# Performance work log

Hardware: AMD Instinct MI355X
Metric: run time of the kernel (lower is better)

The kernel has to match this reference:

```python
import jax, jax.numpy as jnp
import numpy as np

N_GAUSS = 2048
FOCAL = 110.0
NEAR = 0.3
EPS = 1e-4  # matches EPS in source (scale.abs() + EPS)
LOWPASS = 0.3 / (FOCAL * FOCAL)  # low-pass dilation in camera-plane units


def _q2r(q):
    # q: (N,4) wxyz -> (N,3,3) rotation matrices (normalized quaternions)
    q = q / (jnp.linalg.norm(q, axis=-1, keepdims=True) + 1e-8)
    w, x, y, z = q[:, 0], q[:, 1], q[:, 2], q[:, 3]
    R = jnp.stack([
        jnp.stack([1 - 2 * (y * y + z * z), 2 * (x * y - w * z), 2 * (x * z + w * y)], -1),
        jnp.stack([2 * (x * y + w * z), 1 - 2 * (x * x + z * z), 2 * (y * z - w * x)], -1),
        jnp.stack([2 * (x * z - w * y), 2 * (y * z + w * x), 1 - 2 * (x * x + y * y)], -1),
    ], axis=1)
    return R


def _forward(pos, rgb, opa, quat, scale, w2c, tran, H, W):
    # world -> camera
    cam = pos @ w2c.T + tran                      # (N,3)
    z = cam[:, 2]
    valid = z > NEAR
    zs = jnp.where(valid, z, 1.0)
    u = cam[:, 0] / zs                            # camera-plane x
    v = cam[:, 1] / zs                            # camera-plane y

    # 3D covariance: RSSR^T  (scale_activation='abs')
    R = _q2r(quat)
    s = jnp.abs(scale) + EPS
    RS = R * s[:, None, :]                        # R @ diag(s)
    cov3 = jnp.einsum('nij,nkj->nik', RS, RS)     # (N,3,3)
    # rotate into camera frame: W cov3 W^T
    covc = jnp.einsum('ij,njk,lk->nil', w2c, cov3, w2c)

    # perspective Jacobian, 2D covariance = J covc J^T
    iz = 1.0 / zs
    zero = jnp.zeros_like(iz)
    J = jnp.stack([
        jnp.stack([iz, zero, -u * iz], -1),
        jnp.stack([zero, iz, -v * iz], -1),
    ], axis=1)                                    # (N,2,3)
    cov2 = jnp.einsum('nij,njk,nlk->nil', J, covc, J)
    a = cov2[:, 0, 0] + LOWPASS
    b = cov2[:, 0, 1]
    c = cov2[:, 1, 1] + LOWPASS
    det = jnp.maximum(a * c - b * b, 1e-12)
    ia, ib, ic = c / det, -b / det, a / det       # inverse 2x2 cov

    # global front-to-back depth sort (invalid gaussians pushed to the end)
    order = jnp.argsort(jnp.where(valid, z, jnp.inf))
    u, v = u[order], v[order]
    ia, ib, ic = ia[order], ib[order], ic[order]
    opa_s = opa[order]
    rgb_s = rgb[order]
    valid_s = valid[order]

    # pixel centers in camera-plane units
    upix = (jnp.arange(W, dtype=jnp.float32) - W / 2 + 0.5) / FOCAL
    vpix = (jnp.arange(H, dtype=jnp.float32) - H / 2 + 0.5) / FOCAL
    gu, gv = jnp.meshgrid(upix, vpix)             # (H,W) each
    gu = gu.reshape(-1)                           # (P,)
    gv = gv.reshape(-1)

    dx = gu[None, :] - u[:, None]                 # (N,P)
    dy = gv[None, :] - v[:, None]
    power = -0.5 * (ia[:, None] * dx * dx + 2.0 * ib[:, None] * dx * dy + ic[:, None] * dy * dy)
    gw = jnp.exp(jnp.minimum(power, 0.0))
    alpha = jnp.clip(jax.nn.sigmoid(opa_s)[:, None] * gw, 0.0, 0.99)
    alpha = jnp.where(valid_s[:, None], alpha, 0.0)

    # transmittance via exclusive cumsum of log(1-alpha), front-to-back
    lt = jnp.log1p(-alpha)
    logT = jnp.cumsum(lt, axis=0) - lt            # exclusive prefix sum
    wgt = alpha * jnp.exp(logT)                   # (N,P) compositing weights
    img = jnp.einsum('np,nc->pc', wgt, jax.nn.sigmoid(rgb_s))
    return img.reshape(H, W, 3)


def setup_inputs() -> dict:
    key = jax.random.key(0)
    k = jax.random.split(key, 8)
    H, W = 128, 128
    # positions in front of the (near-identity) camera, inside the frustum
    z = jax.random.uniform(k[0], (N_GAUSS,), minval=2.0, maxval=6.0)
    uv = jax.random.uniform(k[1], (N_GAUSS, 2), minval=-0.5, maxval=0.5)
    pos = jnp.stack([uv[:, 0] * z, uv[:, 1] * z, z], axis=-1)
    rgb = jax.random.normal(k[2], (N_GAUSS, 3), dtype=jnp.float32)
    opa = jax.random.normal(k[3], (N_GAUSS,), dtype=jnp.float32)
    quat = jax.random.normal(k[4], (N_GAUSS, 4), dtype=jnp.float32)
    scale = jax.random.uniform(k[5], (N_GAUSS, 3), minval=0.005, maxval=0.05)
    # small random rotation (Rodrigues) so w2c is a valid, near-identity rotation
    axis = jax.random.normal(k[6], (3,))
    axis = axis / (jnp.linalg.norm(axis) + 1e-8)
    th = 0.05
    K = jnp.array([[0.0, -axis[2], axis[1]],
                   [axis[2], 0.0, -axis[0]],
                   [-axis[1], axis[0], 0.0]], dtype=jnp.float32)
    w2c = jnp.eye(3, dtype=jnp.float32) + jnp.sin(th) * K + (1 - jnp.cos(th)) * (K @ K)
    tran = 0.01 * jax.random.normal(k[7], (3,), dtype=jnp.float32)
    return {"pos": pos, "rgb": rgb, "opa": opa, "quat": quat, "scale": scale,
            "w2c": w2c, "tran": tran, "H": H, "W": W}


def reference(pos, rgb, opa, quat, scale, w2c, tran, H, W):
    return _forward(pos, rgb, opa, quat, scale, w2c, tran, H, W)
```

## Files before the change

kernel.cpp:

```cpp
#include <hip/hip_runtime.h>
#include <hip/hip_fp16.h>
#include <math.h>

#define NG 2048
#define HH 128
#define WW 128
#define FOCAL 110.0f
#define NEARP 0.3f
#define EPSS 1e-4f
#define LOWPASS (0.3f / (110.0f * 110.0f))
#define L2E 1.4426950408889634f
#define INV_L2E 0.6931471805599453f
#define LN_INV_ACUT 11.512925465f

#define NSEG 16

#define EXP2F(x) __builtin_amdgcn_exp2f(x)
#define LOG2F(x) __builtin_amdgcn_logf(x)
#define RCPF(x)  __builtin_amdgcn_rcpf(x)
#define SQRTF(x) __builtin_amdgcn_sqrtf(x)

struct Proj {
    float u, v, a, b, c, z, osig;
    bool valid;
};

__device__ __forceinline__ Proj project_one(int g,
        const float* __restrict__ pos, const float* __restrict__ opa,
        const float* __restrict__ quat, const float* __restrict__ scale,
        const float* __restrict__ w2c, const float* __restrict__ tran) {
    float W00 = w2c[0], W01 = w2c[1], W02 = w2c[2];
    float W10 = w2c[3], W11 = w2c[4], W12 = w2c[5];
    float W20 = w2c[6], W21 = w2c[7], W22 = w2c[8];

    float px = pos[g * 3 + 0], py = pos[g * 3 + 1], pz = pos[g * 3 + 2];
    float cx = W00 * px + W01 * py + W02 * pz + tran[0];
    float cy = W10 * px + W11 * py + W12 * pz + tran[1];
    float cz = W20 * px + W21 * py + W22 * pz + tran[2];

    bool valid = cz > NEARP;
    float iz = valid ? RCPF(cz) : 1.0f;
    float u = cx * iz;
    float v = cy * iz;

    float qw = quat[g * 4 + 0], qx = quat[g * 4 + 1], qy = quat[g * 4 + 2], qz = quat[g * 4 + 3];
    float qq = qw * qw + qx * qx + qy * qy + qz * qz;
    float inv = RCPF(SQRTF(qq) + 1e-8f);
    qw *= inv; qx *= inv; qy *= inv; qz *= inv;
    float R00 = 1.0f - 2.0f * (qy * qy + qz * qz);
    float R01 = 2.0f * (qx * qy - qw * qz);
    float R02 = 2.0f * (qx * qz + qw * qy);
    float R10 = 2.0f * (qx * qy + qw * qz);
    float R11 = 1.0f - 2.0f * (qx * qx + qz * qz);
    float R12 = 2.0f * (qy * qz - qw * qx);
    float R20 = 2.0f * (qx * qz - qw * qy);
    float R21 = 2.0f * (qy * qz + qw * qx);
    float R22 = 1.0f - 2.0f * (qx * qx + qy * qy);

    float s0 = fabsf(scale[g * 3 + 0]) + EPSS;
    float s1 = fabsf(scale[g * 3 + 1]) + EPSS;
    float s2 = fabsf(scale[g * 3 + 2]) + EPSS;

    float A00 = R00 * s0, A01 = R01 * s1, A02 = R02 * s2;
    float A10 = R10 * s0, A11 = R11 * s1, A12 = R12 * s2;
    float A20 = R20 * s0, A21 = R21 * s1, A22 = R22 * s2;
    float C00 = A00 * A00 + A01 * A01 + A02 * A02;
    float C01 = A00 * A10 + A01 * A11 + A02 * A12;
    float C02 = A00 * A20 + A01 * A21 + A02 * A22;
    float C11 = A10 * A10 + A11 * A11 + A12 * A12;
    float C12 = A10 * A20 + A11 * A21 + A12 * A22;
    float C22 = A20 * A20 + A21 * A21 + A22 * A22;

    float B00 = W00 * C00 + W01 * C01 + W02 * C02;
    float B01 = W00 * C01 + W01 * C11 + W02 * C12;
    float B02 = W00 * C02 + W01 * C12 + W02 * C22;
    float B10 = W10 * C00 + W11 * C01 + W12 * C02;
    float B11 = W10 * C01 + W11 * C11 + W12 * C12;
    float B12 = W10 * C02 + W11 * C12 + W12 * C22;
    float B20 = W20 * C00 + W21 * C01 + W22 * C02;
    float B21 = W20 * C01 + W21 * C11 + W22 * C12;
    float B22 = W20 * C02 + W21 * C12 + W22 * C22;
    float M00 = B00 * W00 + B01 * W01 + B02 * W02;
    float M01 = B00 * W10 + B01 * W11 + B02 * W12;
    float M02 = B00 * W20 + B01 * W21 + B02 * W22;
    float M11 = B10 * W10 + B11 * W11 + B12 * W12;
    float M12 = B10 * W20 + B11 * W21 + B12 * W22;
    float M22 = B20 * W20 + B21 * W21 + B22 * W22;

    float iz2 = iz * iz;
    Proj r;
    r.a = iz2 * (M00 - 2.0f * u * M02 + u * u * M22) + LOWPASS;
    r.b = iz2 * (M01 - v * M02 - u * M12 + u * v * M22);
    r.c = iz2 * (M11 - 2.0f * v * M12 + v * v * M22) + LOWPASS;
    r.u = u; r.v = v; r.z = cz; r.valid = valid;
    float e = EXP2F(-opa[g] * L2E);
    r.osig = valid ? RCPF(1.0f + e) : 0.0f;
    return r;
}

__device__ __forceinline__ float fast_sigmoid(float x) {
    return RCPF(1.0f + EXP2F(-x * L2E));
}

__global__ __launch_bounds__(1024) void splat_fused(const float* __restrict__ pos,
                                                    const float* __restrict__ rgb,
                                                    const float* __restrict__ opa,
                                                    const float* __restrict__ quat,
                                                    const float* __restrict__ scale,
                                                    const float* __restrict__ w2c,
                                                    const float* __restrict__ tran,
                                                    float* __restrict__ out) {
    __shared__ unsigned long long zk[NG];
    __shared__ unsigned short srt[NG];
    __shared__ float4 ppA[NG];
    __shared__ float4 ppB[NG];
    __shared__ float4 seg[NSEG][64];
    __shared__ int cnt;

    int t = threadIdx.x;
    int lane = t & 63;
    int wave = t >> 6;
    int bx = blockIdx.x & 15, by = blockIdx.x >> 4;

    float cu = ((float)(bx * 8) + 3.5f - 63.5f) / FOCAL;
    float cv = ((float)(by * 8) + 3.5f - 63.5f) / FOCAL;
    const float hw = 3.5f / FOCAL;

    if (t == 0) cnt = 0;
    __syncthreads();

    #pragma unroll
    for (int part = 0; part < 2; ++part) {
        int g = t + part * 1024;
        Proj P = project_one(g, pos, opa, quat, scale, w2c, tran);
        float e = EXP2F(-opa[g] * L2E);
        float tau = 2.0f * (LN_INV_ACUT - LOG2F(1.0f + e) * INV_L2E);
        bool survive = false;
        if (P.valid && tau > 0.0f) {
            float ru = SQRTF(tau * P.a);
            float rv = SQRTF(tau * P.c);
            survive = (fabsf(P.u - cu) <= ru + hw) && (fabsf(P.v - cv) <= rv + hw);
        }
        if (survive) {
            int s = atomicAdd(&cnt, 1);
            zk[s] = ((unsigned long long)__float_as_uint(P.z) << 32) | (unsigned int)g;
        }
    }
    __syncthreads();
    int L = cnt;

    for (int i = t; i < L; i += 1024) {
        unsigned long long ki = zk[i];
        int r = 0;
        #pragma unroll 4
        for (int j = 0; j < L; ++j) r += (zk[j] < ki) ? 1 : 0;
        srt[r] = (unsigned short)(ki & 0xffffu);
    }
    __syncthreads();

    for (int i = t; i < L; i += 1024) {
        int g = srt[i];
        Proj P = project_one(g, pos, opa, quat, scale, w2c, tran);
        float det = fmaxf(P.a * P.c - P.b * P.b, 1e-12f);
        float idet = RCPF(det);
        float Af = -0.5f * L2E * (P.c * idet);
        float Bf =  L2E * (P.b * idet);
        float Cf = -0.5f * L2E * (P.a * idet);
        float rr = fast_sigmoid(rgb[g * 3 + 0]);
        float gg = fast_sigmoid(rgb[g * 3 + 1]);
        float bb = fast_sigmoid(rgb[g * 3 + 2]);
        union { __half2 h; float f; } prg, pb;
        prg.h = __floats2half2_rn(rr, gg);
        pb.h  = __floats2half2_rn(bb, 0.0f);
        ppA[i] = make_float4(P.u, P.v, Af, Bf);
        ppB[i] = make_float4(Cf, P.osig, prg.f, pb.f);
    }
    __syncthreads();

    int px = bx * 8 + (lane & 7);
    int py = by * 8 + (lane >> 3);
    float gu = ((float)px - 63.5f) / FOCAL;
    float gv = ((float)py - 63.5f) / FOCAL;

    int s = (L * wave) >> 4;
    int e = (L * (wave + 1)) >> 4;

    float T = 1.0f, cr = 0.0f, cg = 0.0f, cb = 0.0f;
    for (int i = s; i < e; ++i) {
        float4 q0 = ppA[i];
        float4 q1 = ppB[i];

        float dx = gu - q0.x;
        float dy = gv - q0.y;
        float t1 = fmaf(q0.w, dy, q0.z * dx);
        float p  = fmaf(t1, dx, q1.x * (dy * dy));
        p = fminf(p, 0.0f);
        float gw = EXP2F(p);
        float alpha = fminf(q1.y * gw, 0.99f);
        float w = alpha * T;

        union { float f; __half2 h; } crg, cbb;
        crg.f = q1.z; cbb.f = q1.w;
        float2 rg = __half22float2(crg.h);
        float bch = __low2float(cbb.h);

        cr = fmaf(w, rg.x, cr);
        cg = fmaf(w, rg.y, cg);
        cb = fmaf(w, bch, cb);
        T = fmaf(-alpha, T, T);
    }
    seg[wave][lane] = make_float4(cr, cg, cb, T);
    __syncthreads();

    if (t < 64) {
        float Tt = 1.0f, r = 0.0f, g = 0.0f, b = 0.0f;
        #pragma unroll
        for (int sgi = 0; sgi < NSEG; ++sgi) {
            float4 v = seg[sgi][t];
            r = fmaf(Tt, v.x, r);
            g = fmaf(Tt, v.y, g);
            b = fmaf(Tt, v.z, b);
            Tt *= v.w;
        }
        int p = py * WW + px;
        out[p * 3 + 0] = r;
        out[p * 3 + 1] = g;
        out[p * 3 + 2] = b;
    }
}

extern "C" void kernel_launch(void* const* d_in, const int* in_sizes, int n_in,
                              void* d_out, int out_size, void* d_ws, size_t ws_size,
                              hipStream_t stream) {
    const float* pos   = (const float*)d_in[0];
    const float* rgb   = (const float*)d_in[1];
    const float* opa   = (const float*)d_in[2];
    const float* quat  = (const float*)d_in[3];
    const float* scale = (const float*)d_in[4];
    const float* w2c   = (const float*)d_in[5];
    const float* tran  = (const float*)d_in[6];
    float* out = (float*)d_out;

    splat_fused<<<(HH * WW) / 64, 1024, 0, stream>>>(pos, rgb, opa, quat, scale, w2c, tran, out);
}
```

Measured before the change: 12.64 us.

## Compute projected 2D covariance directly and parallelize depth rank sort

The 2D covariance is now built directly from the product of the perspective Jacobian, w2c, rotation and scale, instead of forming the full 3D covariance and rotating it. The per-gaussian conic parameters are computed once, during culling, and written to shared memory at the atomic slot, so surviving gaussians are no longer projected a second time. The rank sort now has 16 lanes share each key and sum their counts with shuffles, which spreads the quadratic comparison work when few gaussians survive. The cost is an extra indirection in the render loop: each iteration first reads the sorted slot from srt, then loads that gaussian's parameters.

```diff
diff --git a/kernel.cpp b/kernel.cpp
--- a/kernel.cpp
+++ b/kernel.cpp
@@ -18,85 +18,6 @@
 #define EXP2F(x) __builtin_amdgcn_exp2f(x)
 #define LOG2F(x) __builtin_amdgcn_logf(x)
 #define RCPF(x)  __builtin_amdgcn_rcpf(x)
-#define SQRTF(x) __builtin_amdgcn_sqrtf(x)
-
-struct Proj {
-    float u, v, a, b, c, z, osig;
-    bool valid;
-};
-
-__device__ __forceinline__ Proj project_one(int g,
-        const float* __restrict__ pos, const float* __restrict__ opa,
-        const float* __restrict__ quat, const float* __restrict__ scale,
-        const float* __restrict__ w2c, const float* __restrict__ tran) {
-    float W00 = w2c[0], W01 = w2c[1], W02 = w2c[2];
-    float W10 = w2c[3], W11 = w2c[4], W12 = w2c[5];
-    float W20 = w2c[6], W21 = w2c[7], W22 = w2c[8];
-
-    float px = pos[g * 3 + 0], py = pos[g * 3 + 1], pz = pos[g * 3 + 2];
-    float cx = W00 * px + W01 * py + W02 * pz + tran[0];
-    float cy = W10 * px + W11 * py + W12 * pz + tran[1];
-    float cz = W20 * px + W21 * py + W22 * pz + tran[2];
-
-    bool valid = cz > NEARP;
-    float iz = valid ? RCPF(cz) : 1.0f;
-    float u = cx * iz;
-    float v = cy * iz;
-
-    float qw = quat[g * 4 + 0], qx = quat[g * 4 + 1], qy = quat[g * 4 + 2], qz = quat[g * 4 + 3];
-    float qq = qw * qw + qx * qx + qy * qy + qz * qz;
-    float inv = RCPF(SQRTF(qq) + 1e-8f);
-    qw *= inv; qx *= inv; qy *= inv; qz *= inv;
-    float R00 = 1.0f - 2.0f * (qy * qy + qz * qz);
-    float R01 = 2.0f * (qx * qy - qw * qz);
-    float R02 = 2.0f * (qx * qz + qw * qy);
-    float R10 = 2.0f * (qx * qy + qw * qz);
-    float R11 = 1.0f - 2.0f * (qx * qx + qz * qz);
-    float R12 = 2.0f * (qy * qz - qw * qx);
-    float R20 = 2.0f * (qx * qz - qw * qy);
-    float R21 = 2.0f * (qy * qz + qw * qx);
-    float R22 = 1.0f - 2.0f * (qx * qx + qy * qy);
-
-    float s0 = fabsf(scale[g * 3 + 0]) + EPSS;
-    float s1 = fabsf(scale[g * 3 + 1]) + EPSS;
-    float s2 = fabsf(scale[g * 3 + 2]) + EPSS;
-
-    float A00 = R00 * s0, A01 = R01 * s1, A02 = R02 * s2;
-    float A10 = R10 * s0, A11 = R11 * s1, A12 = R12 * s2;
-    float A20 = R20 * s0, A21 = R21 * s1, A22 = R22 * s2;
-    float C00 = A00 * A00 + A01 * A01 + A02 * A02;
-    float C01 = A00 * A10 + A01 * A11 + A02 * A12;
-    float C02 = A00 * A20 + A01 * A21 + A02 * A22;
-    float C11 = A10 * A10 + A11 * A11 + A12 * A12;
-    float C12 = A10 * A20 + A11 * A21 + A12 * A22;
-    float C22 = A20 * A20 + A21 * A21 + A22 * A22;
-
-    float B00 = W00 * C00 + W01 * C01 + W02 * C02;
-    float B01 = W00 * C01 + W01 * C11 + W02 * C12;
-    float B02 = W00 * C02 + W01 * C12 + W02 * C22;
-    float B10 = W10 * C00 + W11 * C01 + W12 * C02;
-    float B11 = W10 * C01 + W11 * C11 + W12 * C12;
-    float B12 = W10 * C02 + W11 * C12 + W12 * C22;
-    float B20 = W20 * C00 + W21 * C01 + W22 * C02;
-    float B21 = W20 * C01 + W21 * C11 + W22 * C12;
-    float B22 = W20 * C02 + W21 * C12 + W22 * C22;
-    float M00 = B00 * W00 + B01 * W01 + B02 * W02;
-    float M01 = B00 * W10 + B01 * W11 + B02 * W12;
-    float M02 = B00 * W20 + B01 * W21 + B02 * W22;
-    float M11 = B10 * W10 + B11 * W11 + B12 * W12;
-    float M12 = B10 * W20 + B11 * W21 + B12 * W22;
-    float M22 = B20 * W20 + B21 * W21 + B22 * W22;
-
-    float iz2 = iz * iz;
-    Proj r;
-    r.a = iz2 * (M00 - 2.0f * u * M02 + u * u * M22) + LOWPASS;
-    r.b = iz2 * (M01 - v * M02 - u * M12 + u * v * M22);
-    r.c = iz2 * (M11 - 2.0f * v * M12 + v * v * M22) + LOWPASS;
-    r.u = u; r.v = v; r.z = cz; r.valid = valid;
-    float e = EXP2F(-opa[g] * L2E);
-    r.osig = valid ? RCPF(1.0f + e) : 0.0f;
-    return r;
-}
 
 __device__ __forceinline__ float fast_sigmoid(float x) {
     return RCPF(1.0f + EXP2F(-x * L2E));
@@ -105,15 +26,15 @@
 __global__ __launch_bounds__(1024) void splat_fused(const float* __restrict__ pos,
                                                     const float* __restrict__ rgb,
                                                     const float* __restrict__ opa,
-                                                    const float* __restrict__ quat,
+                                                    const float4* __restrict__ quat,
                                                     const float* __restrict__ scale,
                                                     const float* __restrict__ w2c,
                                                     const float* __restrict__ tran,
                                                     float* __restrict__ out) {
     __shared__ unsigned long long zk[NG];
-    __shared__ unsigned short srt[NG];
     __shared__ float4 ppA[NG];
     __shared__ float4 ppB[NG];
+    __shared__ unsigned short srt[NG];
     __shared__ float4 seg[NSEG][64];
     __shared__ int cnt;
 
@@ -129,51 +50,106 @@
     if (t == 0) cnt = 0;
     __syncthreads();
 
+    float W00 = w2c[0], W01 = w2c[1], W02 = w2c[2];
+    float W10 = w2c[3], W11 = w2c[4], W12 = w2c[5];
+    float W20 = w2c[6], W21 = w2c[7], W22 = w2c[8];
+    float t0 = tran[0], t1 = tran[1], t2 = tran[2];
+
     #pragma unroll
     for (int part = 0; part < 2; ++part) {
         int g = t + part * 1024;
-        Proj P = project_one(g, pos, opa, quat, scale, w2c, tran);
+
+        float px = pos[g * 3 + 0], py = pos[g * 3 + 1], pz = pos[g * 3 + 2];
+        float cx = W00 * px + W01 * py + W02 * pz + t0;
+        float cy = W10 * px + W11 * py + W12 * pz + t1;
+        float cz = W20 * px + W21 * py + W22 * pz + t2;
+
+        bool valid = cz > NEARP;
+        float iz = valid ? RCPF(cz) : 1.0f;
+        float u = cx * iz;
+        float v = cy * iz;
+
         float e = EXP2F(-opa[g] * L2E);
+        float osig = RCPF(1.0f + e);
         float tau = 2.0f * (LN_INV_ACUT - LOG2F(1.0f + e) * INV_L2E);
-        bool survive = false;
-        if (P.valid && tau > 0.0f) {
-            float ru = SQRTF(tau * P.a);
-            float rv = SQRTF(tau * P.c);
-            survive = (fabsf(P.u - cu) <= ru + hw) && (fabsf(P.v - cv) <= rv + hw);
+
+        float k00 = iz * (W00 - u * W20), k01 = iz * (W01 - u * W21), k02 = iz * (W02 - u * W22);
+        float k10 = iz * (W10 - v * W20), k11 = iz * (W11 - v * W21), k12 = iz * (W12 - v * W22);
+
+        float4 q = quat[g];
+        float qw = q.x, qx = q.y, qy = q.z, qz = q.w;
+        float qq = qw * qw + qx * qx + qy * qy + qz * qz;
+        float inv = RCPF(__builtin_amdgcn_sqrtf(qq) + 1e-8f);
+        qw *= inv; qx *= inv; qy *= inv; qz *= inv;
+        float R00 = 1.0f - 2.0f * (qy * qy + qz * qz);
+        float R01 = 2.0f * (qx * qy - qw * qz);
+        float R02 = 2.0f * (qx * qz + qw * qy);
+        float R10 = 2.0f * (qx * qy + qw * qz);
+        float R11 = 1.0f - 2.0f * (qx * qx + qz * qz);
+        float R12 = 2.0f * (qy * qz - qw * qx);
+        float R20 = 2.0f * (qx * qz - qw * qy);
+        float R21 = 2.0f * (qy * qz + qw * qx);
+        float R22 = 1.0f - 2.0f * (qx * qx + qy * qy);
+
+        float s0 = fabsf(scale[g * 3 + 0]) + EPSS;
+        float s1 = fabsf(scale[g * 3 + 1]) + EPSS;
+        float s2 = fabsf(scale[g * 3 + 2]) + EPSS;
+
+        float g00 = (k00 * R00 + k01 * R10 + k02 * R20) * s0;
+        float g01 = (k00 * R01 + k01 * R11 + k02 * R21) * s1;
+        float g02 = (k00 * R02 + k01 * R12 + k02 * R22) * s2;
+        float g10 = (k10 * R00 + k11 * R10 + k12 * R20) * s0;
+        float g11 = (k10 * R01 + k11 * R11 + k12 * R21) * s1;
+        float g12 = (k10 * R02 + k11 * R12 + k12 * R22) * s2;
+
+        float a = g00 * g00 + g01 * g01 + g02 * g02 + LOWPASS;
+        float c = g10 * g10 + g11 * g11 + g12 * g12 + LOWPASS;
+
+        float du = fmaxf(fabsf(u - cu) - hw, 0.0f);
+        float dv = fmaxf(fabsf(v - cv) - hw, 0.0f);
+        bool survive = valid && (tau > 0.0f) &&
+                       (du * du <= tau * a) && (dv * dv <= tau * c);
+
+        if (survive) {
+            float b = g00 * g10 + g01 * g11 + g02 * g12;
+            float det = fmaxf(a * c - b * b, 1e-12f);
+            float idet = RCPF(det);
+            float Af = -0.5f * L2E * (c * idet);
+            float Bf =  L2E * (b * idet);
+            float Cf = -0.5f * L2E * (a * idet);
+            int s = atomicAdd(&cnt, 1);
+            zk[s] = ((unsigned long long)__float_as_uint(cz) << 32) | (unsigned int)g;
+            ppA[s] = make_float4(u, v, Af, Bf);
+            ppB[s] = make_float4(Cf, osig, 0.0f, 0.0f);
         }
-        if (survive) {
-            int s = atomicAdd(&cnt, 1);
-            zk[s] = ((unsigned long long)__float_as_uint(P.z) << 32) | (unsigned int)g;
+    }
+    __syncthreads();
+    int L = cnt;
+
+    {
+        int sub = t & 15;
+        for (int i = t >> 4; i < L; i += 64) {
+            unsigned long long ki = zk[i];
+            int r = 0;
+            for (int j = sub; j < L; j += 16) r += (zk[j] < ki) ? 1 : 0;
+            r += __shfl_xor(r, 1);
+            r += __shfl_xor(r, 2);
+            r += __shfl_xor(r, 4);
+            r += __shfl_xor(r, 8);
+            if (sub == 0) srt[r] = (unsigned short)i;
         }
     }
-    __syncthreads();
-    int L = cnt;
 
     for (int i = t; i < L; i += 1024) {
-        unsigned long long ki = zk[i];
-        int r = 0;
-        #pragma unroll 4
-        for (int j = 0; j < L; ++j) r += (zk[j] < ki) ? 1 : 0;
-        srt[r] = (unsigned short)(ki & 0xffffu);
-    }
-    __syncthreads();
-
-    for (int i = t; i < L; i += 1024) {
-        int g = srt[i];
-        Proj P = project_one(g, pos, opa, quat, scale, w2c, tran);
-        float det = fmaxf(P.a * P.c - P.b * P.b, 1e-12f);
-        float idet = RCPF(det);
-        float Af = -0.5f * L2E * (P.c * idet);
-        float Bf =  L2E * (P.b * idet);
-        float Cf = -0.5f * L2E * (P.a * idet);
+        int g = (int)(zk[i] & 0xffffu);
         float rr = fast_sigmoid(rgb[g * 3 + 0]);
         float gg = fast_sigmoid(rgb[g * 3 + 1]);
         float bb = fast_sigmoid(rgb[g * 3 + 2]);
         union { __half2 h; float f; } prg, pb;
         prg.h = __floats2half2_rn(rr, gg);
         pb.h  = __floats2half2_rn(bb, 0.0f);
-        ppA[i] = make_float4(P.u, P.v, Af, Bf);
-        ppB[i] = make_float4(Cf, P.osig, prg.f, pb.f);
+        ppB[i].z = prg.f;
+        ppB[i].w = pb.f;
     }
     __syncthreads();
 
@@ -187,13 +163,14 @@
 
     float T = 1.0f, cr = 0.0f, cg = 0.0f, cb = 0.0f;
     for (int i = s; i < e; ++i) {
-        float4 q0 = ppA[i];
-        float4 q1 = ppB[i];
+        int slot = srt[i];
+        float4 q0 = ppA[slot];
+        float4 q1 = ppB[slot];
 
         float dx = gu - q0.x;
         float dy = gv - q0.y;
-        float t1 = fmaf(q0.w, dy, q0.z * dx);
-        float p  = fmaf(t1, dx, q1.x * (dy * dy));
+        float t1v = fmaf(q0.w, dy, q0.z * dx);
+        float p   = fmaf(t1v, dx, q1.x * (dy * dy));
         p = fminf(p, 0.0f);
         float gw = EXP2F(p);
         float alpha = fminf(q1.y * gw, 0.99f);
@@ -201,11 +178,11 @@
 
         union { float f; __half2 h; } crg, cbb;
         crg.f = q1.z; cbb.f = q1.w;
-        float2 rg = __half22float2(crg.h);
+        float2 rgv = __half22float2(crg.h);
         float bch = __low2float(cbb.h);
 
-        cr = fmaf(w, rg.x, cr);
-        cg = fmaf(w, rg.y, cg);
+        cr = fmaf(w, rgv.x, cr);
+        cg = fmaf(w, rgv.y, cg);
         cb = fmaf(w, bch, cb);
         T = fmaf(-alpha, T, T);
     }
@@ -235,7 +212,7 @@
     const float* pos   = (const float*)d_in[0];
     const float* rgb   = (const float*)d_in[1];
     const float* opa   = (const float*)d_in[2];
-    const float* quat  = (const float*)d_in[3];
+    const float4* quat = (const float4*)d_in[3];
     const float* scale = (const float*)d_in[4];
     const float* w2c   = (const float*)d_in[5];
     const float* tran  = (const float*)d_in[6];
```

Result: faster. 11.30 us (-10.6%).
